# Kernel optimization log

Hardware: AMD Instinct MI355X
Metric: run time of the kernel (lower is better)

Reference implementation:

```python
import jax, jax.numpy as jnp
import numpy as np

B = 32768        # batch
COORD = 64       # entorhinal coordinate dim
DG = 2048        # dentate gyrus dim
CA3 = 256        # CA3 dim
CA1 = 256        # CA1 dim
K_ACTIVE = max(1, int(DG * 0.04))   # = 81, DG top-k sparsity
SETTLE_STEPS = 5
GAIN = 0.7
SIGMA = 2.0      # ca3_distance_sigma
N_EPISODES = 64  # ca3_max_episodes
EC_TAU = 0.5
LN_EPS = 1e-5
COS_EPS = 1e-8


def _build_w_recurrent():
    """Hebbian outer-product weights gated by anatomical distance mask (numpy, deterministic)."""
    rng = np.random.default_rng(0)
    theta = np.linspace(0.0, np.pi, CA3)
    pos = np.stack([3.0 * np.cos(theta),
                    4.0 + np.sin(theta),
                    rng.standard_normal(CA3) * 0.8], axis=-1)
    pos = pos + rng.standard_normal(pos.shape) * 0.15
    diff = pos[None, :, :] - pos[:, None, :]
    dist = np.sqrt((diff ** 2).sum(-1) + 1e-8)
    mask = np.exp(-dist / SIGMA)                       # [CA3, CA3] distance gate
    P = rng.standard_normal((N_EPISODES, CA3)).astype(np.float32)
    P = P / (np.linalg.norm(P, axis=1, keepdims=True) + 1e-8)
    W = P.T @ P                                        # Hebbian pattern storage
    np.fill_diagonal(W, 0.0)
    W = W * mask
    return jnp.asarray(W, dtype=jnp.float32)


def setup_inputs() -> dict:
    key = jax.random.key(0)
    ks = jax.random.split(key, 16)
    def lin(k, out_d, in_d):
        s = 1.0 / np.sqrt(in_d)
        return jax.random.uniform(k, (out_d, in_d), jnp.float32, -s, s)
    return {
        "coords":   jax.random.normal(ks[0], (B, COORD), jnp.float32),
        # EC layernorm
        "ec_gamma": jnp.ones((COORD,), jnp.float32),
        "ec_beta":  jnp.zeros((COORD,), jnp.float32),
        # DG perforant path + layernorm
        "W_pp":     lin(ks[1], DG, COORD),
        "b_pp":     jnp.zeros((DG,), jnp.float32),
        "dg_gamma": jnp.ones((DG,), jnp.float32),
        "dg_beta":  jnp.zeros((DG,), jnp.float32),
        # CA3
        "W_mossy":  lin(ks[2], CA3, DG),
        "W_rec":    _build_w_recurrent(),
        "W_sc":     lin(ks[3], CA1, CA3),
        "b_sc":     jnp.zeros((CA1,), jnp.float32),
        # CA1 comparator
        "W_ta":     lin(ks[4], CA1, COORD),
        "b_ta":     jnp.zeros((CA1,), jnp.float32),
        "W_cs":     lin(ks[5], CA1, CA1),
        "W_cd":     lin(ks[6], CA1, CA1),
        "W_og":     lin(ks[7], CA1, CA1),
        "b_og":     jnp.zeros((CA1,), jnp.float32),
    }


def _layernorm(x, gamma, beta):
    mu = jnp.mean(x, axis=-1, keepdims=True)
    var = jnp.mean(jnp.square(x - mu), axis=-1, keepdims=True)
    return (x - mu) * jax.lax.rsqrt(var + LN_EPS) * gamma + beta


def reference(coords, ec_gamma, ec_beta, W_pp, b_pp, dg_gamma, dg_beta,
              W_mossy, W_rec, W_sc, b_sc, W_ta, b_ta, W_cs, W_cd, W_og, b_og):
    # --- EntorhinalCortex: short-term buffer (no-grad EMA from zero init) + layernorm ---
    buf = EC_TAU * 0.0 + (1.0 - EC_TAU) * jax.lax.stop_gradient(jnp.mean(coords, axis=0))
    ec = _layernorm(coords + 0.1 * buf[None, :], ec_gamma, ec_beta)          # [B, COORD]

    # --- DentateGyrus: relu -> layernorm -> top-k sparsification (scatter) ---
    proj = _layernorm(jax.nn.relu(ec @ W_pp.T + b_pp), dg_gamma, dg_beta)    # [B, DG]
    vals, idx = jax.lax.top_k(proj, K_ACTIVE)                                # [B, K]
    rows = jnp.arange(proj.shape[0])[:, None]
    dg = jnp.zeros_like(proj).at[rows, idx].set(vals)                        # sparse code

    # --- CA3AttractorNetwork: mossy cue + recurrent attractor settle ---
    cue = dg @ W_mossy.T                                                     # [B, CA3]
    state = cue
    for _ in range(SETTLE_STEPS):
        state = jnp.tanh(GAIN * (state @ W_rec.T) + (1.0 - GAIN) * cue)
    ca1_input = state @ W_sc.T + b_sc                                        # [B, CA1]

    # --- CA1Comparator: novelty-gated mix of direct EC path and schaffer input ---
    direct = ec @ W_ta.T + b_ta                                              # [B, CA1]
    s_proj = ca1_input @ W_cs.T
    d_proj = direct @ W_cd.T
    s_n = jnp.maximum(jnp.linalg.norm(s_proj, axis=-1), COS_EPS)
    d_n = jnp.maximum(jnp.linalg.norm(d_proj, axis=-1), COS_EPS)
    cos_sim = jnp.sum(s_proj * d_proj, axis=-1) / (s_n * d_n)
    novelty = jnp.clip(1.0 - cos_sim, 0.0, 1.0)                              # [B]
    gate = novelty[:, None]
    combined = gate * direct + (1.0 - gate) * ca1_input
    ca1_output = jnp.tanh(combined @ W_og.T + b_og)                          # [B, CA1]
    return ca1_output, novelty
```

## Files before the change

kernel.cpp:

```cpp
#include <hip/hip_runtime.h>
#include <hip/hip_bf16.h>
#include <math.h>

#define B_N 32768
#define COORD 64
#define DG 2048
#define CA 256
#define K_ACT 81
#define SETTLE_STEPS 5
#define GAIN 0.7f
#define LN_EPS 1e-5f
#define COS_EPS 1e-8f

__device__ __forceinline__ float wave_sum(float v) {
#pragma unroll
  for (int d = 1; d < 64; d <<= 1) v += __shfl_xor(v, d);
  return v;
}

__device__ __forceinline__ float dot4(float4 a, float4 b) {
  return a.x * b.x + a.y * b.y + a.z * b.z + a.w * b.w;
}

__device__ __forceinline__ void fma4(float4& a, float s, float4 w) {
  a.x += s * w.x; a.y += s * w.y; a.z += s * w.z; a.w += s * w.w;
}

__device__ __forceinline__ float fast_tanh(float x) {
  float e = __expf(2.0f * x);
  return 1.0f - 2.0f / (e + 1.0f);
}

__device__ __forceinline__ unsigned int okey(float f) {
  unsigned int u = __float_as_uint(f);
  return (u & 0x80000000u) ? ~u : (u | 0x80000000u);
}

__global__ void colsum_kernel(const float* __restrict__ coords,
                              float* __restrict__ colsum) {
  int tid = threadIdx.x;
  int col = tid & 63;
  int rg = tid >> 6;
  float s = 0.f;
  int base = blockIdx.x * 128;
#pragma unroll 4
  for (int i = 0; i < 32; ++i) {
    int r = base + rg + i * 4;
    s += coords[r * COORD + col];
  }
  __shared__ float sh[256];
  sh[tid] = s;
  __syncthreads();
  if (tid < 64) {
    float t = sh[tid] + sh[tid + 64] + sh[tid + 128] + sh[tid + 192];
    atomicAdd(&colsum[tid], t);
  }
}

__global__ void transpose_any(const float* __restrict__ S,
                              float* __restrict__ T, int R, int C) {
  int idx = blockIdx.x * 256 + threadIdx.x;
  if (idx < R * C) {
    int r = idx / C, c = idx - r * C;
    T[c * R + r] = S[r * C + c];
  }
}

__global__ void fuse_mm(const float* __restrict__ A, const float* __restrict__ BT,
                        const float* __restrict__ bvec, float* __restrict__ FT,
                        float* __restrict__ cvec) {
  __shared__ float brow[256];
  int in = blockIdx.x, out = threadIdx.x;
  brow[out] = BT[in * 256 + out];
  __syncthreads();
  const float* arow = A + out * 256;
  float acc = 0.f;
#pragma unroll 4
  for (int k = 0; k < 256; ++k) acc += arow[k] * brow[k];
  FT[in * 256 + out] = acc;
  if (in == 0) {
    float b = 0.f;
#pragma unroll 4
    for (int k = 0; k < 256; ++k) b += arow[k] * bvec[k];
    cvec[out] = b;
  }
}

__global__ __launch_bounds__(512, 4) void mega1(
    const float* __restrict__ coords, const float* __restrict__ colsum,
    const float* __restrict__ ec_gamma, const float* __restrict__ ec_beta,
    const float* __restrict__ W_ppT, const float* __restrict__ b_pp,
    const float* __restrict__ dg_gamma, const float* __restrict__ dg_beta,
    const float* __restrict__ WmT, float* __restrict__ cue_g) {
  __shared__ __align__(16) float proj_s[8][DG];
  __shared__ __align__(16) float ec_s[8][COORD];
  __shared__ unsigned int hist[8][256];
  __shared__ float psum_s[8][8], psq_s[8][8];
  __shared__ int sel_s[8][88];

  const int w = threadIdx.x >> 6;
  const int l = threadIdx.x & 63;
  const int row0 = blockIdx.x * 8;

  {
    int row = row0 + w;
    float x = coords[row * COORD + l] + (0.05f / (float)B_N) * colsum[l];
    float mu = wave_sum(x) * (1.f / 64.f);
    float d = x - mu;
    float var = wave_sum(d * d) * (1.f / 64.f);
    ec_s[w][l] = d * rsqrtf(var + LN_EPS) * ec_gamma[l] + ec_beta[l];
  }
  __syncthreads();

  {
    float4 acc[8];
#pragma unroll
    for (int r = 0; r < 8; ++r) acc[r] = make_float4(0.f, 0.f, 0.f, 0.f);
    const float4* wp4 = reinterpret_cast<const float4*>(W_ppT);
    const int cbase = 64 * w + l;
    for (int kg = 0; kg < 16; ++kg) {
      float4 w40 = wp4[(4 * kg + 0) * 512 + cbase];
      float4 w41 = wp4[(4 * kg + 1) * 512 + cbase];
      float4 w42 = wp4[(4 * kg + 2) * 512 + cbase];
      float4 w43 = wp4[(4 * kg + 3) * 512 + cbase];
#pragma unroll
      for (int r = 0; r < 8; ++r) {
        float4 e4 = reinterpret_cast<const float4*>(ec_s[r])[kg];
        fma4(acc[r], e4.x, w40);
        fma4(acc[r], e4.y, w41);
        fma4(acc[r], e4.z, w42);
        fma4(acc[r], e4.w, w43);
      }
    }
    float4 bp = reinterpret_cast<const float4*>(b_pp)[cbase];
#pragma unroll
    for (int r = 0; r < 8; ++r) {
      float4 h;
      h.x = fmaxf(acc[r].x + bp.x, 0.f);
      h.y = fmaxf(acc[r].y + bp.y, 0.f);
      h.z = fmaxf(acc[r].z + bp.z, 0.f);
      h.w = fmaxf(acc[r].w + bp.w, 0.f);
      reinterpret_cast<float4*>(proj_s[r])[cbase] = h;
      float ps = wave_sum(h.x + h.y + h.z + h.w);
      float pq = wave_sum(dot4(h, h));
      if (l == 0) { psum_s[w][r] = ps; psq_s[w][r] = pq; }
    }
  }
  __syncthreads();

  float mu2, rs2;
  {
    float s = 0.f, q = 0.f;
#pragma unroll
    for (int w2 = 0; w2 < 8; ++w2) { s += psum_s[w2][w]; q += psq_s[w2][w]; }
    mu2 = s * (1.f / (float)DG);
    float var = q * (1.f / (float)DG) - mu2 * mu2;
    rs2 = rsqrtf(var + LN_EPS);
  }
  unsigned int key[32];
#pragma unroll 4
  for (int i = 0; i < 32; ++i) {
    int j = i * 64 + l;
    float v = (proj_s[w][j] - mu2) * rs2 * dg_gamma[j] + dg_beta[j];
    proj_s[w][j] = v;
    key[i] = okey(v);
  }

  unsigned int prefix = 0, rem = K_ACT;
#pragma unroll 1
  for (int pass = 0; pass < 4; ++pass) {
    int sh = 24 - 8 * pass;
#pragma unroll
    for (int b = l; b < 256; b += 64) hist[w][b] = 0;
#pragma unroll 4
    for (int i = 0; i < 32; ++i) {
      unsigned int k = key[i];
      bool ok = (pass == 0) || ((k >> (sh + 8)) == prefix);
      if (ok) atomicAdd(&hist[w][(k >> sh) & 255u], 1u);
    }
    unsigned int h0 = hist[w][4 * l + 0], h1 = hist[w][4 * l + 1];
    unsigned int h2 = hist[w][4 * l + 2], h3 = hist[w][4 * l + 3];
    unsigned int own = h0 + h1 + h2 + h3;
    unsigned int inc = own;
#pragma unroll
    for (int d = 1; d < 64; d <<= 1) {
      unsigned int v = __shfl_down(inc, d);
      if (l + d < 64) inc += v;
    }
    unsigned int cnt = inc - own;
    unsigned int pk = 0;
    {
      unsigned int hb;
      hb = h3; if (cnt < rem && rem <= cnt + hb) pk = ((rem - cnt) << 8) | (unsigned)(4 * l + 3); cnt += hb;
      hb = h2; if (cnt < rem && rem <= cnt + hb) pk = ((rem - cnt) << 8) | (unsigned)(4 * l + 2); cnt += hb;
      hb = h1; if (cnt < rem && rem <= cnt + hb) pk = ((rem - cnt) << 8) | (unsigned)(4 * l + 1); cnt += hb;
      hb = h0; if (cnt < rem && rem <= cnt + hb) pk = ((rem - cnt) << 8) | (unsigned)(4 * l + 0); cnt += hb;
    }
#pragma unroll
    for (int d = 1; d < 64; d <<= 1) pk |= __shfl_xor(pk, d);
    prefix = (prefix << 8) | (pk & 255u);
    rem = pk >> 8;
  }
  const unsigned int Tkey = prefix;
  const unsigned int rem_final = rem;

  const unsigned long long below = (1ull << l) - 1ull;
  int basec = 0;
  unsigned int eq_seen = 0;
  for (int i = 0; i < 32; ++i) {
    int j = i * 64 + l;
    unsigned int k = key[i];
    bool gt = k > Tkey;
    bool eq = (k == Tkey);
    unsigned long long em = __ballot(eq);
    unsigned int eq_before = eq_seen + (unsigned)__popcll(em & below);
    bool sel = gt || (eq && (eq_before < rem_final));
    unsigned long long sm = __ballot(sel);
    int pos = basec + (int)__popcll(sm & below);
    if (sel) sel_s[w][pos] = j;
    basec += (int)__popcll(sm);
    eq_seen += (unsigned)__popcll(em);
  }

  float4 c4 = make_float4(0.f, 0.f, 0.f, 0.f);
  const float4* wm4 = reinterpret_cast<const float4*>(WmT);
  for (int k = 0; k < K_ACT; ++k) {
    int j = sel_s[w][k];
    float v = proj_s[w][j];
    fma4(c4, v, wm4[j * 64 + l]);
  }
  reinterpret_cast<float4*>(cue_g)[(size_t)(row0 + w) * 64 + l] = c4;
}

__global__ __launch_bounds__(256, 4) void mega2(
    const float* __restrict__ coords, const float* __restrict__ colsum,
    const float* __restrict__ ec_gamma, const float* __restrict__ ec_beta,
    const float* __restrict__ cue_g, const float* __restrict__ W_recT,
    const float* __restrict__ F1T, const float* __restrict__ c1,
    const float* __restrict__ F2T, const float* __restrict__ c2,
    const float* __restrict__ F3T, const float* __restrict__ c3,
    const float* __restrict__ F4T, const float* __restrict__ c4v,
    const float* __restrict__ b_og, float* __restrict__ out) {
  __shared__ __align__(16) float st_s[32][CA];
  __shared__ __align__(16) float ec_s[32][COORD];

  const int w = threadIdx.x >> 6;
  const int l = threadIdx.x & 63;
  const int row0 = blockIdx.x * 32 + w * 8;

#pragma unroll 1
  for (int r = 0; r < 8; ++r) {
    int row = row0 + r;
    float x = coords[row * COORD + l] + (0.05f / (float)B_N) * colsum[l];
    float mu = wave_sum(x) * (1.f / 64.f);
    float d = x - mu;
    float var = wave_sum(d * d) * (1.f / 64.f);
    ec_s[w * 8 + r][l] = d * rsqrtf(var + LN_EPS) * ec_gamma[l] + ec_beta[l];
  }

  float4 cu[8];
#pragma unroll
  for (int r = 0; r < 8; ++r) {
    cu[r] = reinterpret_cast<const float4*>(cue_g)[(size_t)(row0 + r) * 64 + l];
    reinterpret_cast<float4*>(st_s[w * 8 + r])[l] = cu[r];
  }

  float4 acc[8];

  {
    const float4* wr4 = reinterpret_cast<const float4*>(W_recT);
#pragma unroll 1
    for (int it = 0; it < SETTLE_STEPS; ++it) {
#pragma unroll
      for (int r = 0; r < 8; ++r) acc[r] = make_float4(0.f, 0.f, 0.f, 0.f);
#pragma unroll 2
      for (int jg = 0; jg < 64; ++jg) {
        float4 w40 = wr4[(4 * jg + 0) * 64 + l];
        float4 w41 = wr4[(4 * jg + 1) * 64 + l];
        float4 w42 = wr4[(4 * jg + 2) * 64 + l];
        float4 w43 = wr4[(4 * jg + 3) * 64 + l];
#pragma unroll
        for (int r = 0; r < 8; ++r) {
          float4 s4 = reinterpret_cast<const float4*>(st_s[w * 8 + r])[jg];
          fma4(acc[r], s4.x, w40);
          fma4(acc[r], s4.y, w41);
          fma4(acc[r], s4.z, w42);
          fma4(acc[r], s4.w, w43);
        }
      }
#pragma unroll
      for (int r = 0; r < 8; ++r) {
        float4 ns;
        ns.x = fast_tanh(GAIN * acc[r].x + (1.f - GAIN) * cu[r].x);
        ns.y = fast_tanh(GAIN * acc[r].y + (1.f - GAIN) * cu[r].y);
        ns.z = fast_tanh(GAIN * acc[r].z + (1.f - GAIN) * cu[r].z);
        ns.w = fast_tanh(GAIN * acc[r].w + (1.f - GAIN) * cu[r].w);
        reinterpret_cast<float4*>(st_s[w * 8 + r])[l] = ns;
      }
    }
  }

  float4 dpr[8];
  {
    const float4* f4 = reinterpret_cast<const float4*>(F2T);
#pragma unroll
    for (int r = 0; r < 8; ++r) dpr[r] = make_float4(0.f, 0.f, 0.f, 0.f);
#pragma unroll 2
    for (int kg = 0; kg < 16; ++kg) {
      float4 w40 = f4[(4 * kg + 0) * 64 + l];
      float4 w41 = f4[(4 * kg + 1) * 64 + l];
      float4 w42 = f4[(4 * kg + 2) * 64 + l];
      float4 w43 = f4[(4 * kg + 3) * 64 + l];
#pragma unroll
      for (int r = 0; r < 8; ++r) {
        float4 e4 = reinterpret_cast<const float4*>(ec_s[w * 8 + r])[kg];
        fma4(dpr[r], e4.x, w40);
        fma4(dpr[r], e4.y, w41);
        fma4(dpr[r], e4.z, w42);
        fma4(dpr[r], e4.w, w43);
      }
    }
    float4 cb = reinterpret_cast<const float4*>(c2)[l];
#pragma unroll
    for (int r = 0; r < 8; ++r) {
      dpr[r].x += cb.x; dpr[r].y += cb.y; dpr[r].z += cb.z; dpr[r].w += cb.w;
    }
  }

  {
    const float4* f4 = reinterpret_cast<const float4*>(F1T);
#pragma unroll
    for (int r = 0; r < 8; ++r) acc[r] = make_float4(0.f, 0.f, 0.f, 0.f);
#pragma unroll 2
    for (int jg = 0; jg < 64; ++jg) {
      float4 w40 = f4[(4 * jg + 0) * 64 + l];
      float4 w41 = f4[(4 * jg + 1) * 64 + l];
      float4 w42 = f4[(4 * jg + 2) * 64 + l];
      float4 w43 = f4[(4 * jg + 3) * 64 + l];
#pragma unroll
      for (int r = 0; r < 8; ++r) {
        float4 s4 = reinterpret_cast<const float4*>(st_s[w * 8 + r])[jg];
        fma4(acc[r], s4.x, w40);
        fma4(acc[r], s4.y, w41);
        fma4(acc[r], s4.z, w42);
        fma4(acc[r], s4.w, w43);
      }
    }
    float4 cb = reinterpret_cast<const float4*>(c1)[l];
#pragma unroll
    for (int r = 0; r < 8; ++r) {
      acc[r].x += cb.x; acc[r].y += cb.y; acc[r].z += cb.z; acc[r].w += cb.w;
    }
  }

  float nov[8];
#pragma unroll 1
  for (int r = 0; r < 8; ++r) {
    float sd = wave_sum(dot4(acc[r], dpr[r]));
    float sn = wave_sum(dot4(acc[r], acc[r]));
    float dn = wave_sum(dot4(dpr[r], dpr[r]));
    float s_n = fmaxf(sqrtf(sn), COS_EPS);
    float d_n = fmaxf(sqrtf(dn), COS_EPS);
    nov[r] = fminf(fmaxf(1.f - sd / (s_n * d_n), 0.f), 1.f);
    if (l == 0) out[(size_t)B_N * CA + (row0 + r)] = nov[r];
  }

  {
    const float4* f4 = reinterpret_cast<const float4*>(F4T);
#pragma unroll
    for (int r = 0; r < 8; ++r) dpr[r] = make_float4(0.f, 0.f, 0.f, 0.f);
#pragma unroll 2
    for (int kg = 0; kg < 16; ++kg) {
      float4 w40 = f4[(4 * kg + 0) * 64 + l];
      float4 w41 = f4[(4 * kg + 1) * 64 + l];
      float4 w42 = f4[(4 * kg + 2) * 64 + l];
      float4 w43 = f4[(4 * kg + 3) * 64 + l];
#pragma unroll
      for (int r = 0; r < 8; ++r) {
        float4 e4 = reinterpret_cast<const float4*>(ec_s[w * 8 + r])[kg];
        fma4(dpr[r], e4.x, w40);
        fma4(dpr[r], e4.y, w41);
        fma4(dpr[r], e4.z, w42);
        fma4(dpr[r], e4.w, w43);
      }
    }
    float4 cb = reinterpret_cast<const float4*>(c4v)[l];
#pragma unroll
    for (int r = 0; r < 8; ++r) {
      dpr[r].x += cb.x; dpr[r].y += cb.y; dpr[r].z += cb.z; dpr[r].w += cb.w;
    }
  }

  {
    const float4* f4 = reinterpret_cast<const float4*>(F3T);
#pragma unroll
    for (int r = 0; r < 8; ++r) acc[r] = make_float4(0.f, 0.f, 0.f, 0.f);
#pragma unroll 2
    for (int jg = 0; jg < 64; ++jg) {
      float4 w40 = f4[(4 * jg + 0) * 64 + l];
      float4 w41 = f4[(4 * jg + 1) * 64 + l];
      float4 w42 = f4[(4 * jg + 2) * 64 + l];
      float4 w43 = f4[(4 * jg + 3) * 64 + l];
#pragma unroll
      for (int r = 0; r < 8; ++r) {
        float4 s4 = reinterpret_cast<const float4*>(st_s[w * 8 + r])[jg];
        fma4(acc[r], s4.x, w40);
        fma4(acc[r], s4.y, w41);
        fma4(acc[r], s4.z, w42);
        fma4(acc[r], s4.w, w43);
      }
    }
    float4 cc = reinterpret_cast<const float4*>(c3)[l];
    float4 bo = reinterpret_cast<const float4*>(b_og)[l];
#pragma unroll
    for (int r = 0; r < 8; ++r) {
      float g = nov[r], h = 1.f - nov[r];
      float4 o;
      o.x = fast_tanh(g * dpr[r].x + h * (acc[r].x + cc.x) + bo.x);
      o.y = fast_tanh(g * dpr[r].y + h * (acc[r].y + cc.y) + bo.y);
      o.z = fast_tanh(g * dpr[r].z + h * (acc[r].z + cc.z) + bo.z);
      o.w = fast_tanh(g * dpr[r].w + h * (acc[r].w + cc.w) + bo.w);
      reinterpret_cast<float4*>(out)[(size_t)(row0 + r) * 64 + l] = o;
    }
  }
}

extern "C" void kernel_launch(void* const* d_in, const int* in_sizes, int n_in,
                              void* d_out, int out_size, void* d_ws,
                              size_t ws_size, hipStream_t stream) {
  const float* coords = (const float*)d_in[0];
  const float* ec_gamma = (const float*)d_in[1];
  const float* ec_beta = (const float*)d_in[2];
  const float* W_pp = (const float*)d_in[3];
  const float* b_pp = (const float*)d_in[4];
  const float* dg_gamma = (const float*)d_in[5];
  const float* dg_beta = (const float*)d_in[6];
  const float* W_mossy = (const float*)d_in[7];
  const float* W_rec = (const float*)d_in[8];
  const float* W_sc = (const float*)d_in[9];
  const float* b_sc = (const float*)d_in[10];
  const float* W_ta = (const float*)d_in[11];
  const float* b_ta = (const float*)d_in[12];
  const float* W_cs = (const float*)d_in[13];
  const float* W_cd = (const float*)d_in[14];
  const float* W_og = (const float*)d_in[15];
  const float* b_og = (const float*)d_in[16];
  float* out = (float*)d_out;

  float* ws = (float*)d_ws;
  float* colsum = ws;
  float* WmT    = colsum + 64;
  float* W_ppT  = WmT + 2048 * 256;
  float* W_recT = W_ppT + 64 * 2048;
  float* W_scT  = W_recT + 256 * 256;
  float* W_taT  = W_scT + 256 * 256;
  float* F1T    = W_taT + 64 * 256;
  float* F2T    = F1T + 256 * 256;
  float* F3T    = F2T + 64 * 256;
  float* F4T    = F3T + 256 * 256;
  float* c1     = F4T + 64 * 256;
  float* c2     = c1 + 256;
  float* c3     = c2 + 256;
  float* c4     = c3 + 256;
  float* cue_g  = c4 + 256;

  hipMemsetAsync(colsum, 0, COORD * sizeof(float), stream);
  colsum_kernel<<<256, 256, 0, stream>>>(coords, colsum);
  transpose_any<<<(256 * 2048 + 255) / 256, 256, 0, stream>>>(W_mossy, WmT, 256, 2048);
  transpose_any<<<(2048 * 64 + 255) / 256, 256, 0, stream>>>(W_pp, W_ppT, 2048, 64);
  transpose_any<<<(256 * 256 + 255) / 256, 256, 0, stream>>>(W_rec, W_recT, 256, 256);
  transpose_any<<<(256 * 256 + 255) / 256, 256, 0, stream>>>(W_sc, W_scT, 256, 256);
  transpose_any<<<(256 * 64 + 255) / 256, 256, 0, stream>>>(W_ta, W_taT, 256, 64);

  fuse_mm<<<256, 256, 0, stream>>>(W_cs, W_scT, b_sc, F1T, c1);
  fuse_mm<<<64, 256, 0, stream>>>(W_cd, W_taT, b_ta, F2T, c2);
  fuse_mm<<<256, 256, 0, stream>>>(W_og, W_scT, b_sc, F3T, c3);
  fuse_mm<<<64, 256, 0, stream>>>(W_og, W_taT, b_ta, F4T, c4);

  mega1<<<B_N / 8, 512, 0, stream>>>(coords, colsum, ec_gamma, ec_beta, W_ppT,
                                     b_pp, dg_gamma, dg_beta, WmT, cue_g);
  mega2<<<B_N / 32, 256, 0, stream>>>(coords, colsum, ec_gamma, ec_beta, cue_g,
                                      W_recT, F1T, c1, F2T, c2, F3T, c3, F4T,
                                      c4, b_og, out);
}
```

Baseline: 1.099 ms.

## Run mega2 matmuls on MFMA with split-bf16 (hi/lo) emulation of fp32

Rewrites the CA3 settle loop and CA1 comparator matmuls in mega2 to use bf16 MFMA 16x16x32 instructions. Accuracy is kept close to fp32 by splitting weights and activations into high and low bf16 parts and issuing three MFMAs per tile. Weights are pre-split in global memory and activations are stored split in swizzled LDS. This replaces scalar FMA work with matrix-core throughput, at the cost of three times the MFMA count, extra conversion work and more LDS traffic and synchronisation.

```diff
diff --git a/kernel.cpp b/kernel.cpp
--- a/kernel.cpp
+++ b/kernel.cpp
@@ -12,6 +12,9 @@
 #define LN_EPS 1e-5f
 #define COS_EPS 1e-8f
 
+typedef __attribute__((ext_vector_type(8))) short short8v;
+typedef __attribute__((ext_vector_type(4))) float f32x4;
+
 __device__ __forceinline__ float wave_sum(float v) {
 #pragma unroll
   for (int d = 1; d < 64; d <<= 1) v += __shfl_xor(v, d);
@@ -34,6 +37,15 @@
 __device__ __forceinline__ unsigned int okey(float f) {
   unsigned int u = __float_as_uint(f);
   return (u & 0x80000000u) ? ~u : (u | 0x80000000u);
+}
+
+__device__ __forceinline__ ushort f2bf(float f) {
+  unsigned u = __float_as_uint(f);
+  unsigned r = (u + 0x7FFFu + ((u >> 16) & 1u)) >> 16;
+  return (ushort)r;
+}
+__device__ __forceinline__ float bf2f(ushort h) {
+  return __uint_as_float(((unsigned)h) << 16);
 }
 
 __global__ void colsum_kernel(const float* __restrict__ coords,
@@ -66,23 +78,38 @@
   }
 }
 
-__global__ void fuse_mm(const float* __restrict__ A, const float* __restrict__ BT,
-                        const float* __restrict__ bvec, float* __restrict__ FT,
-                        float* __restrict__ cvec) {
+__global__ void split_bf16(const float* __restrict__ S, ushort* __restrict__ H,
+                           ushort* __restrict__ L, int n) {
+  int i = blockIdx.x * 256 + threadIdx.x;
+  if (i < n) {
+    float v = S[i];
+    ushort h = f2bf(v);
+    H[i] = h;
+    L[i] = f2bf(v - bf2f(h));
+  }
+}
+
+__global__ void fuse_mm_bf16(const float* __restrict__ A,
+                             const float* __restrict__ BT,
+                             const float* __restrict__ bvec,
+                             ushort* __restrict__ Fh, ushort* __restrict__ Fl,
+                             float* __restrict__ cvec, int IN) {
   __shared__ float brow[256];
-  int in = blockIdx.x, out = threadIdx.x;
-  brow[out] = BT[in * 256 + out];
-  __syncthreads();
-  const float* arow = A + out * 256;
+  int in = blockIdx.x, outp = threadIdx.x;
+  brow[outp] = BT[in * 256 + outp];
+  __syncthreads();
+  const float* arow = A + outp * 256;
   float acc = 0.f;
 #pragma unroll 4
   for (int k = 0; k < 256; ++k) acc += arow[k] * brow[k];
-  FT[in * 256 + out] = acc;
+  ushort h = f2bf(acc);
+  Fh[outp * IN + in] = h;
+  Fl[outp * IN + in] = f2bf(acc - bf2f(h));
   if (in == 0) {
     float b = 0.f;
 #pragma unroll 4
     for (int k = 0; k < 256; ++k) b += arow[k] * bvec[k];
-    cvec[out] = b;
+    cvec[outp] = b;
   }
 }
 
@@ -232,195 +259,222 @@
   reinterpret_cast<float4*>(cue_g)[(size_t)(row0 + w) * 64 + l] = c4;
 }
 
-__global__ __launch_bounds__(256, 4) void mega2(
+template <int NKS, int RLEN>
+__device__ __forceinline__ void mm_tiles(
+    const ushort* __restrict__ Bh, const ushort* __restrict__ Bl,
+    const ushort* Ah, const ushort* Al, int w, int lg, int ln,
+    f32x4 acc[2][4]) {
+#pragma unroll
+  for (int ks = 0; ks < NKS; ++ks) {
+    const int k0 = 8 * lg + 32 * ks;
+    short8v ah[2], al[2];
+#pragma unroll
+    for (int mt = 0; mt < 2; ++mt) {
+      int m = mt * 16 + ln;
+      int idx = m * RLEN + (k0 ^ (8 * (m & 7)));
+      ah[mt] = *(const short8v*)&Ah[idx];
+      al[mt] = *(const short8v*)&Al[idx];
+    }
+#pragma unroll
+    for (int nt = 0; nt < 4; ++nt) {
+      int n = ln + 16 * (4 * w + nt);
+      short8v bh = *(const short8v*)&Bh[n * RLEN + k0];
+      short8v bl = *(const short8v*)&Bl[n * RLEN + k0];
+#pragma unroll
+      for (int mt = 0; mt < 2; ++mt) {
+        acc[mt][nt] = __builtin_amdgcn_mfma_f32_16x16x32_bf16(ah[mt], bh, acc[mt][nt], 0, 0, 0);
+        acc[mt][nt] = __builtin_amdgcn_mfma_f32_16x16x32_bf16(al[mt], bh, acc[mt][nt], 0, 0, 0);
+        acc[mt][nt] = __builtin_amdgcn_mfma_f32_16x16x32_bf16(ah[mt], bl, acc[mt][nt], 0, 0, 0);
+      }
+    }
+  }
+}
+
+__global__ __launch_bounds__(256, 3) void mega2(
     const float* __restrict__ coords, const float* __restrict__ colsum,
     const float* __restrict__ ec_gamma, const float* __restrict__ ec_beta,
-    const float* __restrict__ cue_g, const float* __restrict__ W_recT,
-    const float* __restrict__ F1T, const float* __restrict__ c1,
-    const float* __restrict__ F2T, const float* __restrict__ c2,
-    const float* __restrict__ F3T, const float* __restrict__ c3,
-    const float* __restrict__ F4T, const float* __restrict__ c4v,
+    const float* __restrict__ cue_g,
+    const ushort* __restrict__ Wrh, const ushort* __restrict__ Wrl,
+    const ushort* __restrict__ F1h, const ushort* __restrict__ F1l, const float* __restrict__ c1,
+    const ushort* __restrict__ F2h, const ushort* __restrict__ F2l, const float* __restrict__ c2,
+    const ushort* __restrict__ F3h, const ushort* __restrict__ F3l, const float* __restrict__ c3,
+    const ushort* __restrict__ F4h, const ushort* __restrict__ F4l, const float* __restrict__ c4v,
     const float* __restrict__ b_og, float* __restrict__ out) {
-  __shared__ __align__(16) float st_s[32][CA];
-  __shared__ __align__(16) float ec_s[32][COORD];
-
-  const int w = threadIdx.x >> 6;
-  const int l = threadIdx.x & 63;
-  const int row0 = blockIdx.x * 32 + w * 8;
+  __shared__ ushort st_h[32 * 256];
+  __shared__ ushort st_l[32 * 256];
+  __shared__ ushort ec_h[32 * 64];
+  __shared__ ushort ec_l[32 * 64];
+  __shared__ float novp[4][32][3];
+  __shared__ float nov_s[32];
+
+  const int t = threadIdx.x;
+  const int w = t >> 6;
+  const int l = t & 63;
+  const int lg = l >> 4;
+  const int ln = l & 15;
+  const int row0 = blockIdx.x * 32;
 
 #pragma unroll 1
   for (int r = 0; r < 8; ++r) {
-    int row = row0 + r;
-    float x = coords[row * COORD + l] + (0.05f / (float)B_N) * colsum[l];
+    int m = w * 8 + r;
+    float x = coords[(size_t)(row0 + m) * COORD + l] + (0.05f / (float)B_N) * colsum[l];
     float mu = wave_sum(x) * (1.f / 64.f);
     float d = x - mu;
     float var = wave_sum(d * d) * (1.f / 64.f);
-    ec_s[w * 8 + r][l] = d * rsqrtf(var + LN_EPS) * ec_gamma[l] + ec_beta[l];
-  }
-
-  float4 cu[8];
-#pragma unroll
-  for (int r = 0; r < 8; ++r) {
-    cu[r] = reinterpret_cast<const float4*>(cue_g)[(size_t)(row0 + r) * 64 + l];
-    reinterpret_cast<float4*>(st_s[w * 8 + r])[l] = cu[r];
-  }
-
-  float4 acc[8];
+    float e = d * rsqrtf(var + LN_EPS) * ec_gamma[l] + ec_beta[l];
+    ushort h = f2bf(e);
+    int idx = m * 64 + (l ^ (8 * (m & 7)));
+    ec_h[idx] = h;
+    ec_l[idx] = f2bf(e - bf2f(h));
+  }
 
   {
-    const float4* wr4 = reinterpret_cast<const float4*>(W_recT);
+    int r = t >> 3;
+    int c0 = (t & 7) * 32;
+#pragma unroll
+    for (int cc = 0; cc < 32; cc += 8) {
+      int c = c0 + cc;
+      const float* src = &cue_g[(size_t)(row0 + r) * CA + c];
+      short8v vh, vl;
+#pragma unroll
+      for (int j = 0; j < 8; ++j) {
+        float v = src[j];
+        ushort h = f2bf(v);
+        vh[j] = (short)h;
+        vl[j] = (short)f2bf(v - bf2f(h));
+      }
+      int idx = r * 256 + (c ^ (8 * (r & 7)));
+      *(short8v*)&st_h[idx] = vh;
+      *(short8v*)&st_l[idx] = vl;
+    }
+  }
+
+  float cue_c[2][4][4];
+#pragma unroll
+  for (int mt = 0; mt < 2; ++mt)
+#pragma unroll
+    for (int nt = 0; nt < 4; ++nt)
+#pragma unroll
+      for (int r = 0; r < 4; ++r)
+        cue_c[mt][nt][r] = cue_g[(size_t)(row0 + mt * 16 + lg * 4 + r) * CA +
+                                 ln + 16 * (4 * w + nt)];
+  __syncthreads();
+
 #pragma unroll 1
-    for (int it = 0; it < SETTLE_STEPS; ++it) {
-#pragma unroll
-      for (int r = 0; r < 8; ++r) acc[r] = make_float4(0.f, 0.f, 0.f, 0.f);
-#pragma unroll 2
-      for (int jg = 0; jg < 64; ++jg) {
-        float4 w40 = wr4[(4 * jg + 0) * 64 + l];
-        float4 w41 = wr4[(4 * jg + 1) * 64 + l];
-        float4 w42 = wr4[(4 * jg + 2) * 64 + l];
-        float4 w43 = wr4[(4 * jg + 3) * 64 + l];
-#pragma unroll
-        for (int r = 0; r < 8; ++r) {
-          float4 s4 = reinterpret_cast<const float4*>(st_s[w * 8 + r])[jg];
-          fma4(acc[r], s4.x, w40);
-          fma4(acc[r], s4.y, w41);
-          fma4(acc[r], s4.z, w42);
-          fma4(acc[r], s4.w, w43);
+  for (int it = 0; it < SETTLE_STEPS; ++it) {
+    f32x4 acc[2][4];
+#pragma unroll
+    for (int mt = 0; mt < 2; ++mt)
+#pragma unroll
+      for (int nt = 0; nt < 4; ++nt) acc[mt][nt] = f32x4{0.f, 0.f, 0.f, 0.f};
+    mm_tiles<8, 256>(Wrh, Wrl, st_h, st_l, w, lg, ln, acc);
+    __syncthreads();
+#pragma unroll
+    for (int mt = 0; mt < 2; ++mt)
+#pragma unroll
+      for (int nt = 0; nt < 4; ++nt)
+#pragma unroll
+        for (int r = 0; r < 4; ++r) {
+          float v = fast_tanh(GAIN * acc[mt][nt][r] + (1.f - GAIN) * cue_c[mt][nt][r]);
+          int m = mt * 16 + lg * 4 + r;
+          int n = ln + 16 * (4 * w + nt);
+          int idx = m * 256 + (n ^ (8 * (m & 7)));
+          ushort h = f2bf(v);
+          st_h[idx] = h;
+          st_l[idx] = f2bf(v - bf2f(h));
         }
-      }
-#pragma unroll
-      for (int r = 0; r < 8; ++r) {
-        float4 ns;
-        ns.x = fast_tanh(GAIN * acc[r].x + (1.f - GAIN) * cu[r].x);
-        ns.y = fast_tanh(GAIN * acc[r].y + (1.f - GAIN) * cu[r].y);
-        ns.z = fast_tanh(GAIN * acc[r].z + (1.f - GAIN) * cu[r].z);
-        ns.w = fast_tanh(GAIN * acc[r].w + (1.f - GAIN) * cu[r].w);
-        reinterpret_cast<float4*>(st_s[w * 8 + r])[l] = ns;
-      }
-    }
-  }
-
-  float4 dpr[8];
-  {
-    const float4* f4 = reinterpret_cast<const float4*>(F2T);
-#pragma unroll
-    for (int r = 0; r < 8; ++r) dpr[r] = make_float4(0.f, 0.f, 0.f, 0.f);
-#pragma unroll 2
-    for (int kg = 0; kg < 16; ++kg) {
-      float4 w40 = f4[(4 * kg + 0) * 64 + l];
-      float4 w41 = f4[(4 * kg + 1) * 64 + l];
-      float4 w42 = f4[(4 * kg + 2) * 64 + l];
-      float4 w43 = f4[(4 * kg + 3) * 64 + l];
-#pragma unroll
-      for (int r = 0; r < 8; ++r) {
-        float4 e4 = reinterpret_cast<const float4*>(ec_s[w * 8 + r])[kg];
-        fma4(dpr[r], e4.x, w40);
-        fma4(dpr[r], e4.y, w41);
-        fma4(dpr[r], e4.z, w42);
-        fma4(dpr[r], e4.w, w43);
-      }
-    }
-    float4 cb = reinterpret_cast<const float4*>(c2)[l];
-#pragma unroll
-    for (int r = 0; r < 8; ++r) {
-      dpr[r].x += cb.x; dpr[r].y += cb.y; dpr[r].z += cb.z; dpr[r].w += cb.w;
-    }
-  }
-
-  {
-    const float4* f4 = reinterpret_cast<const float4*>(F1T);
-#pragma unroll
-    for (int r = 0; r < 8; ++r) acc[r] = make_float4(0.f, 0.f, 0.f, 0.f);
-#pragma unroll 2
-    for (int jg = 0; jg < 64; ++jg) {
-      float4 w40 = f4[(4 * jg + 0) * 64 + l];
-      float4 w41 = f4[(4 * jg + 1) * 64 + l];
-      float4 w42 = f4[(4 * jg + 2) * 64 + l];
-      float4 w43 = f4[(4 * jg + 3) * 64 + l];
-#pragma unroll
-      for (int r = 0; r < 8; ++r) {
-        float4 s4 = reinterpret_cast<const float4*>(st_s[w * 8 + r])[jg];
-        fma4(acc[r], s4.x, w40);
-        fma4(acc[r], s4.y, w41);
-        fma4(acc[r], s4.z, w42);
-        fma4(acc[r], s4.w, w43);
-      }
-    }
-    float4 cb = reinterpret_cast<const float4*>(c1)[l];
-#pragma unroll
-    for (int r = 0; r < 8; ++r) {
-      acc[r].x += cb.x; acc[r].y += cb.y; acc[r].z += cb.z; acc[r].w += cb.w;
-    }
-  }
-
-  float nov[8];
-#pragma unroll 1
-  for (int r = 0; r < 8; ++r) {
-    float sd = wave_sum(dot4(acc[r], dpr[r]));
-    float sn = wave_sum(dot4(acc[r], acc[r]));
-    float dn = wave_sum(dot4(dpr[r], dpr[r]));
+    __syncthreads();
+  }
+
+  f32x4 sp[2][4], dp[2][4];
+#pragma unroll
+  for (int mt = 0; mt < 2; ++mt)
+#pragma unroll
+    for (int nt = 0; nt < 4; ++nt) {
+      sp[mt][nt] = f32x4{0.f, 0.f, 0.f, 0.f};
+      dp[mt][nt] = f32x4{0.f, 0.f, 0.f, 0.f};
+    }
+  mm_tiles<8, 256>(F1h, F1l, st_h, st_l, w, lg, ln, sp);
+  mm_tiles<2, 64>(F2h, F2l, ec_h, ec_l, w, lg, ln, dp);
+#pragma unroll
+  for (int nt = 0; nt < 4; ++nt) {
+    int n = ln + 16 * (4 * w + nt);
+    float a1 = c1[n], a2 = c2[n];
+#pragma unroll
+    for (int mt = 0; mt < 2; ++mt)
+#pragma unroll
+      for (int r = 0; r < 4; ++r) {
+        sp[mt][nt][r] += a1;
+        dp[mt][nt][r] += a2;
+      }
+  }
+
+#pragma unroll
+  for (int mt = 0; mt < 2; ++mt)
+#pragma unroll
+    for (int r = 0; r < 4; ++r) {
+      float psd = 0.f, psn = 0.f, pdn = 0.f;
+#pragma unroll
+      for (int nt = 0; nt < 4; ++nt) {
+        psd += sp[mt][nt][r] * dp[mt][nt][r];
+        psn += sp[mt][nt][r] * sp[mt][nt][r];
+        pdn += dp[mt][nt][r] * dp[mt][nt][r];
+      }
+#pragma unroll
+      for (int d = 1; d < 16; d <<= 1) {
+        psd += __shfl_xor(psd, d);
+        psn += __shfl_xor(psn, d);
+        pdn += __shfl_xor(pdn, d);
+      }
+      if (ln == 0) {
+        int m = mt * 16 + lg * 4 + r;
+        novp[w][m][0] = psd;
+        novp[w][m][1] = psn;
+        novp[w][m][2] = pdn;
+      }
+    }
+  __syncthreads();
+  if (t < 32) {
+    float sd = 0.f, sn = 0.f, dn = 0.f;
+#pragma unroll
+    for (int w2 = 0; w2 < 4; ++w2) {
+      sd += novp[w2][t][0];
+      sn += novp[w2][t][1];
+      dn += novp[w2][t][2];
+    }
     float s_n = fmaxf(sqrtf(sn), COS_EPS);
     float d_n = fmaxf(sqrtf(dn), COS_EPS);
-    nov[r] = fminf(fmaxf(1.f - sd / (s_n * d_n), 0.f), 1.f);
-    if (l == 0) out[(size_t)B_N * CA + (row0 + r)] = nov[r];
-  }
+    float nov = fminf(fmaxf(1.f - sd / (s_n * d_n), 0.f), 1.f);
+    nov_s[t] = nov;
+    out[(size_t)B_N * CA + row0 + t] = nov;
+  }
+  __syncthreads();
 
   {
-    const float4* f4 = reinterpret_cast<const float4*>(F4T);
-#pragma unroll
-    for (int r = 0; r < 8; ++r) dpr[r] = make_float4(0.f, 0.f, 0.f, 0.f);
-#pragma unroll 2
-    for (int kg = 0; kg < 16; ++kg) {
-      float4 w40 = f4[(4 * kg + 0) * 64 + l];
-      float4 w41 = f4[(4 * kg + 1) * 64 + l];
-      float4 w42 = f4[(4 * kg + 2) * 64 + l];
-      float4 w43 = f4[(4 * kg + 3) * 64 + l];
-#pragma unroll
-      for (int r = 0; r < 8; ++r) {
-        float4 e4 = reinterpret_cast<const float4*>(ec_s[w * 8 + r])[kg];
-        fma4(dpr[r], e4.x, w40);
-        fma4(dpr[r], e4.y, w41);
-        fma4(dpr[r], e4.z, w42);
-        fma4(dpr[r], e4.w, w43);
-      }
-    }
-    float4 cb = reinterpret_cast<const float4*>(c4v)[l];
-#pragma unroll
-    for (int r = 0; r < 8; ++r) {
-      dpr[r].x += cb.x; dpr[r].y += cb.y; dpr[r].z += cb.z; dpr[r].w += cb.w;
-    }
-  }
-
-  {
-    const float4* f4 = reinterpret_cast<const float4*>(F3T);
-#pragma unroll
-    for (int r = 0; r < 8; ++r) acc[r] = make_float4(0.f, 0.f, 0.f, 0.f);
-#pragma unroll 2
-    for (int jg = 0; jg < 64; ++jg) {
-      float4 w40 = f4[(4 * jg + 0) * 64 + l];
-      float4 w41 = f4[(4 * jg + 1) * 64 + l];
-      float4 w42 = f4[(4 * jg + 2) * 64 + l];
-      float4 w43 = f4[(4 * jg + 3) * 64 + l];
-#pragma unroll
-      for (int r = 0; r < 8; ++r) {
-        float4 s4 = reinterpret_cast<const float4*>(st_s[w * 8 + r])[jg];
-        fma4(acc[r], s4.x, w40);
-        fma4(acc[r], s4.y, w41);
-        fma4(acc[r], s4.z, w42);
-        fma4(acc[r], s4.w, w43);
-      }
-    }
-    float4 cc = reinterpret_cast<const float4*>(c3)[l];
-    float4 bo = reinterpret_cast<const float4*>(b_og)[l];
-#pragma unroll
-    for (int r = 0; r < 8; ++r) {
-      float g = nov[r], h = 1.f - nov[r];
-      float4 o;
-      o.x = fast_tanh(g * dpr[r].x + h * (acc[r].x + cc.x) + bo.x);
-      o.y = fast_tanh(g * dpr[r].y + h * (acc[r].y + cc.y) + bo.y);
-      o.z = fast_tanh(g * dpr[r].z + h * (acc[r].z + cc.z) + bo.z);
-      o.w = fast_tanh(g * dpr[r].w + h * (acc[r].w + cc.w) + bo.w);
-      reinterpret_cast<float4*>(out)[(size_t)(row0 + r) * 64 + l] = o;
+    f32x4 o1[2][4], o2[2][4];
+#pragma unroll
+    for (int mt = 0; mt < 2; ++mt)
+#pragma unroll
+      for (int nt = 0; nt < 4; ++nt) {
+        o1[mt][nt] = f32x4{0.f, 0.f, 0.f, 0.f};
+        o2[mt][nt] = f32x4{0.f, 0.f, 0.f, 0.f};
+      }
+    mm_tiles<8, 256>(F3h, F3l, st_h, st_l, w, lg, ln, o1);
+    mm_tiles<2, 64>(F4h, F4l, ec_h, ec_l, w, lg, ln, o2);
+#pragma unroll
+    for (int nt = 0; nt < 4; ++nt) {
+      int n = ln + 16 * (4 * w + nt);
+      float a3 = c3[n], a4 = c4v[n], bo = b_og[n];
+#pragma unroll
+      for (int mt = 0; mt < 2; ++mt)
+#pragma unroll
+        for (int r = 0; r < 4; ++r) {
+          int m = mt * 16 + lg * 4 + r;
+          float g = nov_s[m];
+          float o = fast_tanh(g * (o2[mt][nt][r] + a4) +
+                              (1.f - g) * (o1[mt][nt][r] + a3) + bo);
+          out[(size_t)(row0 + m) * CA + n] = o;
+        }
     }
   }
 }
@@ -451,35 +505,41 @@
   float* colsum = ws;
   float* WmT    = colsum + 64;
   float* W_ppT  = WmT + 2048 * 256;
-  float* W_recT = W_ppT + 64 * 2048;
-  float* W_scT  = W_recT + 256 * 256;
+  float* W_scT  = W_ppT + 64 * 2048;
   float* W_taT  = W_scT + 256 * 256;
-  float* F1T    = W_taT + 64 * 256;
-  float* F2T    = F1T + 256 * 256;
-  float* F3T    = F2T + 64 * 256;
-  float* F4T    = F3T + 256 * 256;
-  float* c1     = F4T + 64 * 256;
+  float* c1     = W_taT + 64 * 256;
   float* c2     = c1 + 256;
   float* c3     = c2 + 256;
   float* c4     = c3 + 256;
-  float* cue_g  = c4 + 256;
+  ushort* us    = (ushort*)(c4 + 256);
+  ushort* Wrh   = us;
+  ushort* Wrl   = Wrh + 65536;
+  ushort* F1h   = Wrl + 65536;
+  ushort* F1l   = F1h + 65536;
+  ushort* F3h   = F1l + 65536;
+  ushort* F3l   = F3h + 65536;
+  ushort* F2h   = F3l + 65536;
+  ushort* F2l   = F2h + 16384;
+  ushort* F4h   = F2l + 16384;
+  ushort* F4l   = F4h + 16384;
+  float* cue_g  = (float*)(F4l + 16384);
 
   hipMemsetAsync(colsum, 0, COORD * sizeof(float), stream);
   colsum_kernel<<<256, 256, 0, stream>>>(coords, colsum);
   transpose_any<<<(256 * 2048 + 255) / 256, 256, 0, stream>>>(W_mossy, WmT, 256, 2048);
   transpose_any<<<(2048 * 64 + 255) / 256, 256, 0, stream>>>(W_pp, W_ppT, 2048, 64);
-  transpose_any<<<(256 * 256 + 255) / 256, 256, 0, stream>>>(W_rec, W_recT, 256, 256);
   transpose_any<<<(256 * 256 + 255) / 256, 256, 0, stream>>>(W_sc, W_scT, 256, 256);
   transpose_any<<<(256 * 64 + 255) / 256, 256, 0, stream>>>(W_ta, W_taT, 256, 64);
 
-  fuse_mm<<<256, 256, 0, stream>>>(W_cs, W_scT, b_sc, F1T, c1);
-  fuse_mm<<<64, 256, 0, stream>>>(W_cd, W_taT, b_ta, F2T, c2);
-  fuse_mm<<<256, 256, 0, stream>>>(W_og, W_scT, b_sc, F3T, c3);
-  fuse_mm<<<64, 256, 0, stream>>>(W_og, W_taT, b_ta, F4T, c4);
+  split_bf16<<<256, 256, 0, stream>>>(W_rec, Wrh, Wrl, 256 * 256);
+  fuse_mm_bf16<<<256, 256, 0, stream>>>(W_cs, W_scT, b_sc, F1h, F1l, c1, 256);
+  fuse_mm_bf16<<<64, 256, 0, stream>>>(W_cd, W_taT, b_ta, F2h, F2l, c2, 64);
+  fuse_mm_bf16<<<256, 256, 0, stream>>>(W_og, W_scT, b_sc, F3h, F3l, c3, 256);
+  fuse_mm_bf16<<<64, 256, 0, stream>>>(W_og, W_taT, b_ta, F4h, F4l, c4, 64);
 
   mega1<<<B_N / 8, 512, 0, stream>>>(coords, colsum, ec_gamma, ec_beta, W_ppT,
                                      b_pp, dg_gamma, dg_beta, WmT, cue_g);
   mega2<<<B_N / 32, 256, 0, stream>>>(coords, colsum, ec_gamma, ec_beta, cue_g,
-                                      W_recT, F1T, c1, F2T, c2, F3T, c3, F4T,
-                                      c4, b_og, out);
-}
+                                      Wrh, Wrl, F1h, F1l, c1, F2h, F2l, c2,
+                                      F3h, F3l, c3, F4h, F4l, c4, b_og, out);
+}
```

New measurement: 1.185 ms. 1.08x slower.
